# Optimization experiments

Measured on AMD Instinct MI355X. Metric: run time of the kernel, lower is better.

Reference implementation:

```python
import sys
import jax, jax.numpy as jnp
import numpy as np

sys.setrecursionlimit(100000)

MARGIN = 200.0
SAME_MARGIN = 0.0
REL_MARGIN = MARGIN - SAME_MARGIN  # margin - same_margin


def km_algorithm(mp):
    """Faithful numpy port of the repo's recursive Kuhn-Munkres (host-side,
    exactly mirroring the original CPU round-trip). mp: (n, n) float64.
    Returns transport plan T with T[link[y], y] = 1/n for matched pairs."""
    n = mp.shape[0]
    link = np.full(n, -1, dtype=np.int64)
    lx = mp.max(axis=1).astype(np.float64).copy()
    ly = np.zeros(n, dtype=np.float64)
    st = {}

    def dfs(x):
        st['visx'][x] = True
        for y in range(n):
            if st['visy'][y]:
                continue
            tmp = lx[x] + ly[y] - mp[x, y]
            if abs(tmp) < 1e-5:
                st['visy'][y] = True
                if link[y] == -1 or dfs(link[y]):
                    link[y] = x
                    return True
            elif st['sla'][y] + 1e-5 > tmp:
                st['sla'][y] = tmp
        return False

    for x in range(n):
        st['sla'] = np.full(n, 1e10, dtype=np.float64)
        while True:
            st['visx'] = np.zeros(n, dtype=bool)
            st['visy'] = np.zeros(n, dtype=bool)
            if dfs(x):
                break
            d = st['sla'][~st['visy']].min()
            lx[st['visx']] -= d
            ly[st['visy']] += d
            st['sla'][~st['visy']] -= d
    T = np.zeros((n, n), dtype=np.float64)
    for i in range(n):
        if link[i] != -1:
            T[link[i], i] = 1.0 / n
    return T


def sim_label(l1, l2):
    # (n, n) float: 1 where labels equal
    return (l1[:, None] == l2[None, :]).astype(jnp.float32)


def ground_metric(f1, f2, sim):
    # pairwise squared euclidean distances: ||a||^2 - 2 a.b + ||b||^2
    sq1 = jnp.sum(f1 * f1, axis=1)[:, None]
    sq2 = jnp.sum(f2 * f2, axis=1)[None, :]
    d2 = sq1 - 2.0 * (f1 @ f2.T) + sq2
    hinge_gm = jnp.maximum(0.0, SAME_MARGIN + REL_MARGIN - d2)   # negative pairs
    same_gm = jnp.maximum(0.0, d2 - SAME_MARGIN)                 # positive pairs
    return sim * same_gm + (1.0 - sim) * hinge_gm                # mode='both'


def setup_inputs() -> dict:
    key = jax.random.key(0)
    k1, k2, k3, k4 = jax.random.split(key, 4)
    n, d = 128, 8192
    return {
        "inputs_batch1": jax.random.normal(k1, (n, d), dtype=jnp.float32),
        "inputs_batch2": jax.random.normal(k2, (n, d), dtype=jnp.float32),
        "targets_batch1": jax.random.randint(k3, (n,), 0, 16, dtype=jnp.int64) if jax.config.jax_enable_x64 else jax.random.randint(k3, (n,), 0, 16).astype(jnp.int32),
        "targets_batch2": jax.random.randint(k4, (n,), 0, 16, dtype=jnp.int64) if jax.config.jax_enable_x64 else jax.random.randint(k4, (n,), 0, 16).astype(jnp.int32),
    }


def reference(inputs_batch1, inputs_batch2, targets_batch1, targets_batch2):
    sim = sim_label(targets_batch1, targets_batch2)
    GM = ground_metric(inputs_batch1, inputs_batch2, sim)
    # host round-trip for KM assignment, as in the original module
    T = km_algorithm(np.asarray(jax.device_get(GM), dtype=np.float64))
    T = jnp.asarray(T, dtype=jnp.float32)
    loss = jnp.sum(GM * T)
    return loss
```

## Files before the change

### kernel.cpp

```cpp
#include <hip/hip_runtime.h>

#define N 128
#define DIM 8192
#define NN (N * N)
#define ZSPLIT 64
#define NW 16
#define GSTRIDE 130
#define NSTR 65

__device__ __forceinline__ void wave_fence() {
    __threadfence_block();
    __builtin_amdgcn_wave_barrier();
}
__device__ __forceinline__ double embed_key(double v, int j) {
    long long b = __double_as_longlong(v);
    return __longlong_as_double((b & ~127LL) | (long long)j);
}

__global__ __launch_bounds__(256) void d2_partial(const float* __restrict__ A,
                                                  const float* __restrict__ B,
                                                  float* __restrict__ d2p) {
    __shared__ float As[32][68];
    __shared__ float Bk[64][36];
    const int tid = threadIdx.x;
    const int bi = blockIdx.x, bj = blockIdx.y, bz = blockIdx.z;
    const int tx = tid & 15, ty = tid >> 4;
    const int row0 = bi * 32, col0 = bj * 32;
    const int kbase = bz * 128;
    float a00 = 0.f, a01 = 0.f, a10 = 0.f, a11 = 0.f;

    for (int it = 0; it < 2; ++it) {
        const int k0 = kbase + it * 64;
        __syncthreads();
        #pragma unroll
        for (int s = 0; s < 2; ++s) {
            int e = tid + s * 256;
            int r = e >> 4, q = e & 15;
            *(float4*)&As[r][q * 4] = *(const float4*)&A[(row0 + r) * DIM + k0 + q * 4];
        }
        #pragma unroll
        for (int s = 0; s < 2; ++s) {
            int r = tid & 31;
            int kq = (tid >> 5) + s * 8;
            float4 b4 = *(const float4*)&B[(col0 + r) * DIM + k0 + kq * 4];
            Bk[kq * 4 + 0][r] = b4.x;
            Bk[kq * 4 + 1][r] = b4.y;
            Bk[kq * 4 + 2][r] = b4.z;
            Bk[kq * 4 + 3][r] = b4.w;
        }
        __syncthreads();
        #pragma unroll
        for (int kk = 0; kk < 64; kk += 4) {
            float x0[4], x1[4];
            *(float4*)x0 = *(const float4*)&As[2 * ty][kk];
            *(float4*)x1 = *(const float4*)&As[2 * ty + 1][kk];
            float y[4][2];
            #pragma unroll
            for (int q = 0; q < 4; ++q)
                *(float2*)y[q] = *(const float2*)&Bk[kk + q][2 * tx];
            #pragma unroll
            for (int q = 0; q < 4; ++q) {
                float d;
                d = x0[q] - y[q][0]; a00 = fmaf(d, d, a00);
                d = x0[q] - y[q][1]; a01 = fmaf(d, d, a01);
                d = x1[q] - y[q][0]; a10 = fmaf(d, d, a10);
                d = x1[q] - y[q][1]; a11 = fmaf(d, d, a11);
            }
        }
    }
    const int o0 = (row0 + 2 * ty) * N + col0 + 2 * tx;
    float* dst = d2p + bz * NN;
    *(float2*)&dst[o0]     = make_float2(a00, a01);
    *(float2*)&dst[o0 + N] = make_float2(a10, a11);
}

__global__ __launch_bounds__(256) void reduce_gm(const float* __restrict__ d2p,
                                                 const int* __restrict__ t1,
                                                 const int* __restrict__ t2,
                                                 float* __restrict__ gm,
                                                 int* __restrict__ flagarr) {
    __shared__ int bf;
    if (threadIdx.x == 0) bf = 0;
    __syncthreads();
    const int o = blockIdx.x * 256 + threadIdx.x;
    float s0 = 0.f, s1 = 0.f, s2 = 0.f, s3 = 0.f, s4 = 0.f, s5 = 0.f, s6 = 0.f, s7 = 0.f;
    const float* p = d2p + o;
    #pragma unroll
    for (int z = 0; z < ZSPLIT; z += 8) {
        s0 += p[(z + 0) * NN]; s1 += p[(z + 1) * NN];
        s2 += p[(z + 2) * NN]; s3 += p[(z + 3) * NN];
        s4 += p[(z + 4) * NN]; s5 += p[(z + 5) * NN];
        s6 += p[(z + 6) * NN]; s7 += p[(z + 7) * NN];
    }
    float s = ((s0 + s1) + (s2 + s3)) + ((s4 + s5) + (s6 + s7));
    const int i = o >> 7, j = o & 127;
    const int l1 = t1[i], l2 = t2[j];
    const bool same = (l1 == l2);
    float g = same ? fmaxf(s, 0.f) : fmaxf(200.f - s, 0.f);
    gm[o] = g;
    bool bad = (!same && g > 0.f) || l1 < 0 || l1 > 63 || l2 < 0 || l2 > 63;
    unsigned long long m = __ballot(bad);
    if ((threadIdx.x & 63) == 0 && m) atomicOr(&bf, 1);
    __syncthreads();
    if (threadIdx.x == 0) flagarr[blockIdx.x] = bf;
}

__global__ __launch_bounds__(64) void solve_classes(const float* __restrict__ gm,
                                                    const int* __restrict__ flagarr,
                                                    const int* __restrict__ t1,
                                                    const int* __restrict__ t2,
                                                    double* __restrict__ cls_val) {
    __shared__ float ncls[64 * NSTR];
    __shared__ int rowl[64], coll[64];
    __shared__ int rcnt[64], ccnt[64];
    __shared__ int tasks[64];
    __shared__ int clm[64];

    const int lane = threadIdx.x;
    const int l1a = t1[lane] & 63, l1b = t1[lane + 64] & 63;
    const int l2a = t2[lane] & 63, l2b = t2[lane + 64] & 63;
    const int fl  = flagarr[lane];
    rcnt[lane] = 0; ccnt[lane] = 0;
    __syncthreads();
    atomicAdd(&rcnt[l1a], 1); atomicAdd(&rcnt[l1b], 1);
    atomicAdd(&ccnt[l2a], 1); atomicAdd(&ccnt[l2b], 1);
    __syncthreads();
    const bool flag = (__ballot(fl != 0) != 0ull);
    int ntasks;
    {
        int R = rcnt[lane], C = ccnt[lane];
        bool small = (!flag) && (R > 0) && (C > 0) && (R <= 64) && (C <= 64);
        unsigned long long ms = __ballot(small);
        if (small) tasks[__popcll(ms & ((1ull << lane) - 1))] = lane;
        ntasks = (int)__popcll(ms);
    }
    __syncthreads();
    if ((int)blockIdx.x >= ntasks) {
        if (lane == 0) cls_val[blockIdx.x] = 0.0;
        return;
    }
    const int c = tasks[blockIdx.x];

    const unsigned long long mlt = (1ull << lane) - 1;
    unsigned long long b1 = __ballot(l1a == c);
    unsigned long long b2 = __ballot(l1b == c);
    if (l1a == c) rowl[__popcll(b1 & mlt)] = lane;
    if (l1b == c) rowl[__popcll(b1) + __popcll(b2 & mlt)] = lane + 64;
    const int Rn = (int)(__popcll(b1) + __popcll(b2));
    unsigned long long c1 = __ballot(l2a == c);
    unsigned long long c2 = __ballot(l2b == c);
    if (l2a == c) coll[__popcll(c1 & mlt)] = lane;
    if (l2b == c) coll[__popcll(c1) + __popcll(c2 & mlt)] = lane + 64;
    const int Cn = (int)(__popcll(c1) + __popcll(c2));
    __syncthreads();

    const bool T  = (Rn > Cn);
    const int n_  = T ? Cn : Rn;
    const int m_  = T ? Rn : Cn;
    const int tot = n_ * m_;
    for (int e = lane; e < tot; e += 64) {
        int i = e / m_, j = e - i * m_;
        int gr = T ? rowl[j] : rowl[i];
        int gc = T ? coll[i] : coll[j];
        ncls[i * NSTR + j] = gm[gr * N + gc];
    }
    __syncthreads();

    const int W = (m_ <= 16) ? 16 : (m_ <= 32 ? 32 : 64);
    const bool cA = (lane < m_), rA = (lane < n_);

    double u = 0.0;
    if (rA) {
        float mx = 0.f;
        const float* row = &ncls[lane * NSTR];
        for (int j = 0; j < m_; ++j) mx = fmaxf(mx, row[j]);
        u = -(double)mx;
    }
    double v = 1e30;
    for (int i = 0; i < n_; ++i) {
        double ui = __shfl(u, i, 64);
        if (cA) v = fmin(v, -(double)ncls[i * NSTR + lane] - ui);
    }
    if (cA) clm[lane] = 0x7fffffff;
    wave_fence();
    int jc = -1;
    for (int j = 0; j < m_; ++j) {
        double vj = __shfl(v, j, 64);
        if (rA && jc < 0) {
            double s = -(double)ncls[lane * NSTR + j] - u - vj;
            if (s < 1e-7) jc = j;
        }
    }
    if (rA && jc >= 0) atomicMin(&clm[jc], lane);
    wave_fence();
    int p = -1;
    if (cA && clm[lane] != 0x7fffffff) p = clm[lane];
    bool rowm = (rA && jc >= 0 && clm[jc] == lane);

    for (int ir = 0; ir < n_; ++ir) {
        if (__shfl(rowm ? 1 : 0, ir, 64)) continue;
        double minv = 1e30, markD = -1.0, ent = -1.0;
        bool used = false; int way = -2;
        if (rA && lane == ir) ent = 0.0;
        double D = 0.0;
        int i0 = ir, jprev = -1;
        int guard = 2 * m_ + 8;
        while (guard-- > 0) {
            double ui = __shfl(u, i0, 64);
            if (cA && !used) {
                double cand = D - ui - (double)ncls[i0 * NSTR + lane] - v;
                if (cand < minv) { minv = cand; way = jprev; }
            }
            double kd = (cA && !used) ? embed_key(minv, lane) : 1e30;
            for (int o = 1; o < W; o <<= 1) kd = fmin(kd, __shfl_xor(kd, o, 64));
            long long kb = __double_as_longlong(kd);
            int j1 = (int)(kb & 127);
            double Dn = __longlong_as_double(kb & ~127LL);
            if (Dn > 1e29) break;
            D = Dn;
            int i1 = __shfl(p, j1, 64);
            if (i1 < 0) {
                int jj = j1;
                while (true) {
                    int wp = __shfl(way, jj, 64);
                    int pn = (wp < 0) ? ir : __shfl(p, wp, 64);
                    if (cA && lane == jj) p = pn;
                    if (wp < 0) break;
                    jj = wp;
                }
                if (rA && lane == ir) rowm = true;
                break;
            }
            if (cA && lane == j1) { used = true; markD = D; }
            if (rA && lane == i1) ent = D;
            jprev = j1; i0 = i1;
        }
        if (rA && ent   >= 0.0) u += D - ent;
        if (cA && markD >= 0.0) v -= D - markD;
    }

    double val = 0.0;
    if (cA && p >= 0) val = (double)ncls[p * NSTR + lane];
    #pragma unroll
    for (int o = 1; o < 64; o <<= 1) val += __shfl_xor(val, o, 64);
    if (lane == 0) cls_val[blockIdx.x] = val;
}

__global__ __launch_bounds__(1024) void finalize_kernel(const float* __restrict__ gm,
                                                        const int* __restrict__ flagarr,
                                                        const int* __restrict__ t1,
                                                        const int* __restrict__ t2,
                                                        const double* __restrict__ cls_val,
                                                        float* __restrict__ out) {
    __shared__ float gml[N * GSTRIDE];
    __shared__ int lbl1[N], lbl2[N];
    __shared__ int rowlist[N], collist[N];
    __shared__ int rcnt[64], ccnt[64], rstart[65], cstart[65], rcur[64], ccur[64];
    __shared__ int bigtasks[65];
    __shared__ int nbig_s, flag_s;
    __shared__ double ub[N + 1], vbp[N + 1], minvb[N + 1];
    __shared__ int pb[N + 1], wayb[N + 1], usedb[N + 1];
    __shared__ double redv[NW];
    __shared__ int redi[NW];
    __shared__ double big_total, small_sum;
    __shared__ int jfin_s;

    const int tid = threadIdx.x;
    if (tid < 64) { rcnt[tid] = 0; ccnt[tid] = 0; rcur[tid] = 0; ccur[tid] = 0; }
    if (tid == 0) { nbig_s = 0; flag_s = 0; big_total = 0.0; }
    if (tid < N)  { lbl1[tid] = t1[tid]; lbl2[tid] = t2[tid]; }
    __syncthreads();
    if (tid < 64 && flagarr[tid]) atomicOr(&flag_s, 1);
    if (tid < N) {
        atomicAdd(&rcnt[lbl1[tid] & 63], 1);
        atomicAdd(&ccnt[lbl2[tid] & 63], 1);
    }
    double sv = (tid < 64) ? cls_val[tid] : 0.0;
    __syncthreads();
    if (tid < 64) {
        int rs_ = rcnt[tid], cs_ = ccnt[tid];
        #pragma unroll
        for (int o = 1; o < 64; o <<= 1) {
            int tr = __shfl_up(rs_, o, 64);
            int tc = __shfl_up(cs_, o, 64);
            if (tid >= o) { rs_ += tr; cs_ += tc; }
        }
        rstart[tid + 1] = rs_;
        cstart[tid + 1] = cs_;
        if (tid == 0) { rstart[0] = 0; cstart[0] = 0; }
        if (!flag_s) {
            int R = rcnt[tid], C = ccnt[tid];
            bool big = (R > 0) && (C > 0) && ((R > 64) || (C > 64));
            unsigned long long mb = __ballot(big);
            if (big) bigtasks[__popcll(mb & ((1ull << tid) - 1))] = tid;
            if (tid == 0) nbig_s = __popcll(mb);
        } else if (tid == 0) { nbig_s = 1; bigtasks[0] = -1; }
        #pragma unroll
        for (int o = 1; o < 64; o <<= 1) sv += __shfl_xor(sv, o, 64);
        if (tid == 0) small_sum = sv;
    }
    __syncthreads();

    const int nbig = nbig_s;
    if (nbig > 0) {
        if (tid < N) {
            int l1 = lbl1[tid] & 63;
            int p = atomicAdd(&rcur[l1], 1);
            rowlist[rstart[l1] + p] = tid;
            int l2 = lbl2[tid] & 63;
            int q = atomicAdd(&ccur[l2], 1);
            collist[cstart[l2] + q] = tid;
        }
        __syncthreads();
        #pragma unroll
        for (int pch = 0; pch < 16; ++pch) {
            int e = tid + pch * 1024;
            int i = e >> 7, j = e & 127;
            gml[i * GSTRIDE + j] = gm[rowlist[i] * N + collist[j]];
        }
        __syncthreads();

        for (int bt = 0; bt < nbig; ++bt) {
            const int c = bigtasks[bt];
            int Rn, Cn, rs, cs;
            if (c < 0) { Rn = N; Cn = N; rs = 0; cs = 0; }
            else { Rn = rcnt[c]; Cn = ccnt[c]; rs = rstart[c]; cs = cstart[c]; }
            const bool T = (Rn > Cn);
            const int n_ = T ? Cn : Rn, m_ = T ? Rn : Cn;
            const int rstep = T ? 1 : GSTRIDE;
            const int cstep = T ? GSTRIDE : 1;
            const int rb00 = T ? cs : rs * GSTRIDE;
            const int ob00 = T ? rs * GSTRIDE : cs;
            auto cost = [&](int i, int j) -> double {
                return -(double)gml[rb00 + i * rstep + ob00 + j * cstep];
            };
            for (int x = tid; x <= m_; x += 1024) { vbp[x] = 0.0; pb[x] = 0; }
            for (int x = tid; x <= n_; x += 1024) { ub[x] = 0.0; }
            __syncthreads();
            for (int i = 1; i <= n_; ++i) {
                if (tid == 0) pb[0] = i;
                for (int x = tid; x <= m_; x += 1024) { minvb[x] = 1e300; usedb[x] = 0; }
                __syncthreads();
                int j0 = 0;
                int guard = 2 * m_ + 8;
                while (guard-- > 0) {
                    if (tid == 0) usedb[j0] = 1;
                    __syncthreads();
                    const int i0 = pb[j0];
                    double dl = 1e300; int jl = 0;
                    if (tid < m_) {
                        int j = tid + 1;
                        if (!usedb[j]) {
                            double cur = cost(i0 - 1, j - 1) - ub[i0] - vbp[j];
                            if (cur < minvb[j]) { minvb[j] = cur; wayb[j] = j0; }
                            dl = minvb[j]; jl = j;
                        }
                    }
                    double rv = dl; int ri = jl;
                    #pragma unroll
                    for (int o = 32; o > 0; o >>= 1) {
                        double ov = __shfl_down(rv, o, 64);
                        int oi2 = __shfl_down(ri, o, 64);
                        if (ov < rv) { rv = ov; ri = oi2; }
                    }
                    if ((tid & 63) == 0) { redv[tid >> 6] = rv; redi[tid >> 6] = ri; }
                    __syncthreads();
                    if (tid == 0) {
                        double bd = 1e300; int bj = 0;
                        for (int q = 0; q < NW; ++q) if (redv[q] < bd) { bd = redv[q]; bj = redi[q]; }
                        redv[0] = bd; redi[0] = bj;
                    }
                    __syncthreads();
                    const double delta = redv[0];
                    const int j1 = redi[0];
                    if (tid < m_) {
                        int j = tid + 1;
                        if (usedb[j]) { ub[pb[j]] += delta; vbp[j] -= delta; }
                        else          { minvb[j] -= delta; }
                    }
                    if (tid == 0) ub[pb[0]] += delta;
                    __syncthreads();
                    j0 = j1;
                    if (pb[j0] == 0) break;
                }
                if (tid == 0) jfin_s = j0;
                __syncthreads();
                if (tid == 0) {
                    int jj = jfin_s;
                    while (jj) { int jp = wayb[jj]; pb[jj] = pb[jp]; jj = jp; }
                }
                __syncthreads();
            }
            double bl = 0.0;
            if (tid < m_) { int j = tid + 1; if (pb[j] != 0) bl = -cost(pb[j] - 1, j - 1); }
            #pragma unroll
            for (int o = 32; o > 0; o >>= 1) bl += __shfl_down(bl, o, 64);
            if ((tid & 63) == 0) redv[tid >> 6] = bl;
            __syncthreads();
            if (tid == 0) { double s = 0; for (int q = 0; q < NW; ++q) s += redv[q]; big_total += s; }
            __syncthreads();
        }
    }

    if (tid == 0) out[0] = (float)((small_sum + big_total) / (double)N);
}

extern "C" void kernel_launch(void* const* d_in, const int* in_sizes, int n_in,
                              void* d_out, int out_size, void* d_ws, size_t ws_size,
                              hipStream_t stream) {
    const float* A  = (const float*)d_in[0];
    const float* B  = (const float*)d_in[1];
    const int*   t1 = (const int*)d_in[2];
    const int*   t2 = (const int*)d_in[3];
    float* out = (float*)d_out;
    float* d2p = (float*)d_ws;
    float* gm  = (float*)d_ws + ZSPLIT * NN;
    int*   flagarr = (int*)(gm + NN);
    double* cls_val = (double*)(flagarr + 64);

    d2_partial<<<dim3(4, 4, ZSPLIT), 256, 0, stream>>>(A, B, d2p);
    reduce_gm<<<64, 256, 0, stream>>>(d2p, t1, t2, gm, flagarr);
    solve_classes<<<64, 64, 0, stream>>>(gm, flagarr, t1, t2, cls_val);
    finalize_kernel<<<1, 1024, 0, stream>>>(gm, flagarr, t1, t2, cls_val, out);
}
```

Before: 88.80 us.

## Fuse four kernels into one cooperative kernel with grid syncs

```diff
diff --git a/kernel.cpp b/kernel.cpp
--- a/kernel.cpp
+++ b/kernel.cpp
@@ -1,10 +1,14 @@
 #include <hip/hip_runtime.h>
+#include <hip/hip_cooperative_groups.h>
+
+namespace cg = cooperative_groups;
 
 #define N 128
 #define DIM 8192
 #define NN (N * N)
 #define ZSPLIT 64
-#define NW 16
+#define BDIM 512
+#define NWF 8
 #define GSTRIDE 130
 #define NSTR 65
 
@@ -17,255 +21,242 @@
     return __longlong_as_double((b & ~127LL) | (long long)j);
 }
 
-__global__ __launch_bounds__(256) void d2_partial(const float* __restrict__ A,
-                                                  const float* __restrict__ B,
-                                                  float* __restrict__ d2p) {
-    __shared__ float As[32][68];
-    __shared__ float Bk[64][36];
-    const int tid = threadIdx.x;
-    const int bi = blockIdx.x, bj = blockIdx.y, bz = blockIdx.z;
-    const int tx = tid & 15, ty = tid >> 4;
-    const int row0 = bi * 32, col0 = bj * 32;
-    const int kbase = bz * 128;
-    float a00 = 0.f, a01 = 0.f, a10 = 0.f, a11 = 0.f;
-
-    for (int it = 0; it < 2; ++it) {
-        const int k0 = kbase + it * 64;
-        __syncthreads();
-        #pragma unroll
-        for (int s = 0; s < 2; ++s) {
-            int e = tid + s * 256;
-            int r = e >> 4, q = e & 15;
-            *(float4*)&As[r][q * 4] = *(const float4*)&A[(row0 + r) * DIM + k0 + q * 4];
-        }
-        #pragma unroll
-        for (int s = 0; s < 2; ++s) {
-            int r = tid & 31;
-            int kq = (tid >> 5) + s * 8;
-            float4 b4 = *(const float4*)&B[(col0 + r) * DIM + k0 + kq * 4];
-            Bk[kq * 4 + 0][r] = b4.x;
-            Bk[kq * 4 + 1][r] = b4.y;
-            Bk[kq * 4 + 2][r] = b4.z;
-            Bk[kq * 4 + 3][r] = b4.w;
-        }
-        __syncthreads();
-        #pragma unroll
-        for (int kk = 0; kk < 64; kk += 4) {
-            float x0[4], x1[4];
-            *(float4*)x0 = *(const float4*)&As[2 * ty][kk];
-            *(float4*)x1 = *(const float4*)&As[2 * ty + 1][kk];
-            float y[4][2];
-            #pragma unroll
-            for (int q = 0; q < 4; ++q)
-                *(float2*)y[q] = *(const float2*)&Bk[kk + q][2 * tx];
-            #pragma unroll
-            for (int q = 0; q < 4; ++q) {
-                float d;
-                d = x0[q] - y[q][0]; a00 = fmaf(d, d, a00);
-                d = x0[q] - y[q][1]; a01 = fmaf(d, d, a01);
-                d = x1[q] - y[q][0]; a10 = fmaf(d, d, a10);
-                d = x1[q] - y[q][1]; a11 = fmaf(d, d, a11);
-            }
-        }
-    }
-    const int o0 = (row0 + 2 * ty) * N + col0 + 2 * tx;
-    float* dst = d2p + bz * NN;
-    *(float2*)&dst[o0]     = make_float2(a00, a01);
-    *(float2*)&dst[o0 + N] = make_float2(a10, a11);
-}
-
-__global__ __launch_bounds__(256) void reduce_gm(const float* __restrict__ d2p,
-                                                 const int* __restrict__ t1,
-                                                 const int* __restrict__ t2,
-                                                 float* __restrict__ gm,
-                                                 int* __restrict__ flagarr) {
-    __shared__ int bf;
-    if (threadIdx.x == 0) bf = 0;
-    __syncthreads();
-    const int o = blockIdx.x * 256 + threadIdx.x;
-    float s0 = 0.f, s1 = 0.f, s2 = 0.f, s3 = 0.f, s4 = 0.f, s5 = 0.f, s6 = 0.f, s7 = 0.f;
-    const float* p = d2p + o;
-    #pragma unroll
-    for (int z = 0; z < ZSPLIT; z += 8) {
-        s0 += p[(z + 0) * NN]; s1 += p[(z + 1) * NN];
-        s2 += p[(z + 2) * NN]; s3 += p[(z + 3) * NN];
-        s4 += p[(z + 4) * NN]; s5 += p[(z + 5) * NN];
-        s6 += p[(z + 6) * NN]; s7 += p[(z + 7) * NN];
-    }
-    float s = ((s0 + s1) + (s2 + s3)) + ((s4 + s5) + (s6 + s7));
-    const int i = o >> 7, j = o & 127;
-    const int l1 = t1[i], l2 = t2[j];
-    const bool same = (l1 == l2);
-    float g = same ? fmaxf(s, 0.f) : fmaxf(200.f - s, 0.f);
-    gm[o] = g;
-    bool bad = (!same && g > 0.f) || l1 < 0 || l1 > 63 || l2 < 0 || l2 > 63;
-    unsigned long long m = __ballot(bad);
-    if ((threadIdx.x & 63) == 0 && m) atomicOr(&bf, 1);
-    __syncthreads();
-    if (threadIdx.x == 0) flagarr[blockIdx.x] = bf;
-}
-
-__global__ __launch_bounds__(64) void solve_classes(const float* __restrict__ gm,
-                                                    const int* __restrict__ flagarr,
+__global__ __launch_bounds__(BDIM) void mega_kernel(const float* __restrict__ A,
+                                                    const float* __restrict__ B,
                                                     const int* __restrict__ t1,
                                                     const int* __restrict__ t2,
-                                                    double* __restrict__ cls_val) {
-    __shared__ float ncls[64 * NSTR];
-    __shared__ int rowl[64], coll[64];
-    __shared__ int rcnt[64], ccnt[64];
-    __shared__ int tasks[64];
-    __shared__ int clm[64];
-
-    const int lane = threadIdx.x;
-    const int l1a = t1[lane] & 63, l1b = t1[lane + 64] & 63;
-    const int l2a = t2[lane] & 63, l2b = t2[lane + 64] & 63;
-    const int fl  = flagarr[lane];
-    rcnt[lane] = 0; ccnt[lane] = 0;
-    __syncthreads();
-    atomicAdd(&rcnt[l1a], 1); atomicAdd(&rcnt[l1b], 1);
-    atomicAdd(&ccnt[l2a], 1); atomicAdd(&ccnt[l2b], 1);
-    __syncthreads();
-    const bool flag = (__ballot(fl != 0) != 0ull);
-    int ntasks;
-    {
-        int R = rcnt[lane], C = ccnt[lane];
-        bool small = (!flag) && (R > 0) && (C > 0) && (R <= 64) && (C <= 64);
-        unsigned long long ms = __ballot(small);
-        if (small) tasks[__popcll(ms & ((1ull << lane) - 1))] = lane;
-        ntasks = (int)__popcll(ms);
-    }
-    __syncthreads();
-    if ((int)blockIdx.x >= ntasks) {
-        if (lane == 0) cls_val[blockIdx.x] = 0.0;
-        return;
-    }
-    const int c = tasks[blockIdx.x];
-
-    const unsigned long long mlt = (1ull << lane) - 1;
-    unsigned long long b1 = __ballot(l1a == c);
-    unsigned long long b2 = __ballot(l1b == c);
-    if (l1a == c) rowl[__popcll(b1 & mlt)] = lane;
-    if (l1b == c) rowl[__popcll(b1) + __popcll(b2 & mlt)] = lane + 64;
-    const int Rn = (int)(__popcll(b1) + __popcll(b2));
-    unsigned long long c1 = __ballot(l2a == c);
-    unsigned long long c2 = __ballot(l2b == c);
-    if (l2a == c) coll[__popcll(c1 & mlt)] = lane;
-    if (l2b == c) coll[__popcll(c1) + __popcll(c2 & mlt)] = lane + 64;
-    const int Cn = (int)(__popcll(c1) + __popcll(c2));
-    __syncthreads();
-
-    const bool T  = (Rn > Cn);
-    const int n_  = T ? Cn : Rn;
-    const int m_  = T ? Rn : Cn;
-    const int tot = n_ * m_;
-    for (int e = lane; e < tot; e += 64) {
-        int i = e / m_, j = e - i * m_;
-        int gr = T ? rowl[j] : rowl[i];
-        int gc = T ? coll[i] : coll[j];
-        ncls[i * NSTR + j] = gm[gr * N + gc];
-    }
-    __syncthreads();
-
-    const int W = (m_ <= 16) ? 16 : (m_ <= 32 ? 32 : 64);
-    const bool cA = (lane < m_), rA = (lane < n_);
-
-    double u = 0.0;
-    if (rA) {
-        float mx = 0.f;
-        const float* row = &ncls[lane * NSTR];
-        for (int j = 0; j < m_; ++j) mx = fmaxf(mx, row[j]);
-        u = -(double)mx;
-    }
-    double v = 1e30;
-    for (int i = 0; i < n_; ++i) {
-        double ui = __shfl(u, i, 64);
-        if (cA) v = fmin(v, -(double)ncls[i * NSTR + lane] - ui);
-    }
-    if (cA) clm[lane] = 0x7fffffff;
-    wave_fence();
-    int jc = -1;
-    for (int j = 0; j < m_; ++j) {
-        double vj = __shfl(v, j, 64);
-        if (rA && jc < 0) {
-            double s = -(double)ncls[lane * NSTR + j] - u - vj;
-            if (s < 1e-7) jc = j;
-        }
-    }
-    if (rA && jc >= 0) atomicMin(&clm[jc], lane);
-    wave_fence();
-    int p = -1;
-    if (cA && clm[lane] != 0x7fffffff) p = clm[lane];
-    bool rowm = (rA && jc >= 0 && clm[jc] == lane);
-
-    for (int ir = 0; ir < n_; ++ir) {
-        if (__shfl(rowm ? 1 : 0, ir, 64)) continue;
-        double minv = 1e30, markD = -1.0, ent = -1.0;
-        bool used = false; int way = -2;
-        if (rA && lane == ir) ent = 0.0;
-        double D = 0.0;
-        int i0 = ir, jprev = -1;
-        int guard = 2 * m_ + 8;
-        while (guard-- > 0) {
-            double ui = __shfl(u, i0, 64);
-            if (cA && !used) {
-                double cand = D - ui - (double)ncls[i0 * NSTR + lane] - v;
-                if (cand < minv) { minv = cand; way = jprev; }
-            }
-            double kd = (cA && !used) ? embed_key(minv, lane) : 1e30;
-            for (int o = 1; o < W; o <<= 1) kd = fmin(kd, __shfl_xor(kd, o, 64));
-            long long kb = __double_as_longlong(kd);
-            int j1 = (int)(kb & 127);
-            double Dn = __longlong_as_double(kb & ~127LL);
-            if (Dn > 1e29) break;
-            D = Dn;
-            int i1 = __shfl(p, j1, 64);
-            if (i1 < 0) {
-                int jj = j1;
-                while (true) {
-                    int wp = __shfl(way, jj, 64);
-                    int pn = (wp < 0) ? ir : __shfl(p, wp, 64);
-                    if (cA && lane == jj) p = pn;
-                    if (wp < 0) break;
-                    jj = wp;
-                }
-                if (rA && lane == ir) rowm = true;
-                break;
-            }
-            if (cA && lane == j1) { used = true; markD = D; }
-            if (rA && lane == i1) ent = D;
-            jprev = j1; i0 = i1;
-        }
-        if (rA && ent   >= 0.0) u += D - ent;
-        if (cA && markD >= 0.0) v -= D - markD;
-    }
-
-    double val = 0.0;
-    if (cA && p >= 0) val = (double)ncls[p * NSTR + lane];
-    #pragma unroll
-    for (int o = 1; o < 64; o <<= 1) val += __shfl_xor(val, o, 64);
-    if (lane == 0) cls_val[blockIdx.x] = val;
-}
-
-__global__ __launch_bounds__(1024) void finalize_kernel(const float* __restrict__ gm,
-                                                        const int* __restrict__ flagarr,
-                                                        const int* __restrict__ t1,
-                                                        const int* __restrict__ t2,
-                                                        const double* __restrict__ cls_val,
-                                                        float* __restrict__ out) {
-    __shared__ float gml[N * GSTRIDE];
-    __shared__ int lbl1[N], lbl2[N];
-    __shared__ int rowlist[N], collist[N];
-    __shared__ int rcnt[64], ccnt[64], rstart[65], cstart[65], rcur[64], ccur[64];
-    __shared__ int bigtasks[65];
-    __shared__ int nbig_s, flag_s;
+                                                    float* __restrict__ d2p,
+                                                    float* __restrict__ gm,
+                                                    int* __restrict__ flagarr,
+                                                    double* __restrict__ cls_val,
+                                                    float* __restrict__ out) {
+    union Shm {
+        struct { float As[64][36]; float Bk[32][68]; } d2;
+        float ncls[64 * NSTR];
+        float gml[N * GSTRIDE];
+    };
+    __shared__ Shm sh;
+    __shared__ int bf;
+    __shared__ int rowl[64], coll[64], rcnt[64], ccnt[64], tasks64[64], clm[64];
+    __shared__ int lbl1[N], lbl2[N], rowlist[N], collist[N];
+    __shared__ int rstart[65], cstart[65], rcur[64], ccur[64], bigtasks[65];
+    __shared__ int nbig_s, flag_s, jfin_s;
     __shared__ double ub[N + 1], vbp[N + 1], minvb[N + 1];
     __shared__ int pb[N + 1], wayb[N + 1], usedb[N + 1];
-    __shared__ double redv[NW];
-    __shared__ int redi[NW];
+    __shared__ double redv[NWF];
+    __shared__ int redi[NWF];
     __shared__ double big_total, small_sum;
-    __shared__ int jfin_s;
 
     const int tid = threadIdx.x;
+    cg::grid_group grid = cg::this_grid();
+
+    {
+        const int bz = blockIdx.x & 63;
+        const int bi = (blockIdx.x >> 6) & 1;
+        const int bj = (blockIdx.x >> 7) & 1;
+        const int row0 = bi * 64, col0 = bj * 64;
+        const int kbase = bz * 128;
+        const int tx = tid & 15, ty = tid >> 4;
+        const int lr = tid >> 3, lq = tid & 7;
+        float a0[4] = {0.f, 0.f, 0.f, 0.f}, a1[4] = {0.f, 0.f, 0.f, 0.f};
+
+        for (int it = 0; it < 4; ++it) {
+            const int k0 = kbase + it * 32;
+            __syncthreads();
+            *(float4*)&sh.d2.As[lr][lq * 4] = *(const float4*)&A[(row0 + lr) * DIM + k0 + lq * 4];
+            float4 b4 = *(const float4*)&B[(col0 + lr) * DIM + k0 + lq * 4];
+            sh.d2.Bk[lq * 4 + 0][lr] = b4.x;
+            sh.d2.Bk[lq * 4 + 1][lr] = b4.y;
+            sh.d2.Bk[lq * 4 + 2][lr] = b4.z;
+            sh.d2.Bk[lq * 4 + 3][lr] = b4.w;
+            __syncthreads();
+            #pragma unroll
+            for (int kk = 0; kk < 32; kk += 4) {
+                float x0[4], x1[4];
+                *(float4*)x0 = *(const float4*)&sh.d2.As[2 * ty][kk];
+                *(float4*)x1 = *(const float4*)&sh.d2.As[2 * ty + 1][kk];
+                #pragma unroll
+                for (int q = 0; q < 4; ++q) {
+                    float y[4];
+                    *(float4*)y = *(const float4*)&sh.d2.Bk[kk + q][tx * 4];
+                    #pragma unroll
+                    for (int c = 0; c < 4; ++c) {
+                        float d0 = x0[q] - y[c]; a0[c] = fmaf(d0, d0, a0[c]);
+                        float d1 = x1[q] - y[c]; a1[c] = fmaf(d1, d1, a1[c]);
+                    }
+                }
+            }
+        }
+        float* dst = d2p + bz * NN;
+        const int o0 = (row0 + 2 * ty) * N + col0 + tx * 4;
+        *(float4*)&dst[o0]     = *(float4*)a0;
+        *(float4*)&dst[o0 + N] = *(float4*)a1;
+    }
+    grid.sync();
+
+    {
+        if (tid == 0) bf = 0;
+        __syncthreads();
+        const bool active = (blockIdx.x < 64) && (tid < 256);
+        bool bad = false;
+        if (active) {
+            const int o = blockIdx.x * 256 + tid;
+            const float* p = d2p + o;
+            float s0 = 0.f, s1 = 0.f, s2 = 0.f, s3 = 0.f, s4 = 0.f, s5 = 0.f, s6 = 0.f, s7 = 0.f;
+            #pragma unroll
+            for (int z = 0; z < ZSPLIT; z += 8) {
+                s0 += p[(z + 0) * NN]; s1 += p[(z + 1) * NN];
+                s2 += p[(z + 2) * NN]; s3 += p[(z + 3) * NN];
+                s4 += p[(z + 4) * NN]; s5 += p[(z + 5) * NN];
+                s6 += p[(z + 6) * NN]; s7 += p[(z + 7) * NN];
+            }
+            float s = ((s0 + s1) + (s2 + s3)) + ((s4 + s5) + (s6 + s7));
+            const int i = o >> 7, j = o & 127;
+            const int l1 = t1[i], l2 = t2[j];
+            const bool same = (l1 == l2);
+            float g = same ? fmaxf(s, 0.f) : fmaxf(200.f - s, 0.f);
+            gm[o] = g;
+            bad = (!same && g > 0.f) || l1 < 0 || l1 > 63 || l2 < 0 || l2 > 63;
+        }
+        unsigned long long m = __ballot(bad);
+        if ((tid & 63) == 0 && m) atomicOr(&bf, 1);
+        __syncthreads();
+        if (blockIdx.x < 64 && tid == 0) flagarr[blockIdx.x] = bf;
+    }
+    grid.sync();
+
+    if (blockIdx.x < 64 && tid < 64) {
+        const int lane = tid;
+        const int l1a = t1[lane] & 63, l1b = t1[lane + 64] & 63;
+        const int l2a = t2[lane] & 63, l2b = t2[lane + 64] & 63;
+        const int fl  = flagarr[lane];
+        rcnt[lane] = 0; ccnt[lane] = 0;
+        wave_fence();
+        atomicAdd(&rcnt[l1a], 1); atomicAdd(&rcnt[l1b], 1);
+        atomicAdd(&ccnt[l2a], 1); atomicAdd(&ccnt[l2b], 1);
+        wave_fence();
+        const bool flag = (__ballot(fl != 0) != 0ull);
+        int ntasks;
+        {
+            int R = rcnt[lane], C = ccnt[lane];
+            bool small = (!flag) && (R > 0) && (C > 0) && (R <= 64) && (C <= 64);
+            unsigned long long ms = __ballot(small);
+            if (small) tasks64[__popcll(ms & ((1ull << lane) - 1))] = lane;
+            ntasks = (int)__popcll(ms);
+        }
+        wave_fence();
+        const bool have = ((int)blockIdx.x < ntasks);
+        double val = 0.0;
+        if (have) {
+            const int c = tasks64[blockIdx.x];
+            const unsigned long long mlt = (1ull << lane) - 1;
+            unsigned long long b1 = __ballot(l1a == c);
+            unsigned long long b2 = __ballot(l1b == c);
+            if (l1a == c) rowl[__popcll(b1 & mlt)] = lane;
+            if (l1b == c) rowl[__popcll(b1) + __popcll(b2 & mlt)] = lane + 64;
+            const int Rn = (int)(__popcll(b1) + __popcll(b2));
+            unsigned long long c1 = __ballot(l2a == c);
+            unsigned long long c2 = __ballot(l2b == c);
+            if (l2a == c) coll[__popcll(c1 & mlt)] = lane;
+            if (l2b == c) coll[__popcll(c1) + __popcll(c2 & mlt)] = lane + 64;
+            const int Cn = (int)(__popcll(c1) + __popcll(c2));
+            wave_fence();
+
+            const bool T  = (Rn > Cn);
+            const int n_  = T ? Cn : Rn;
+            const int m_  = T ? Rn : Cn;
+            const int tot = n_ * m_;
+            for (int e = lane; e < tot; e += 64) {
+                int i = e / m_, j = e - i * m_;
+                int gr = T ? rowl[j] : rowl[i];
+                int gc = T ? coll[i] : coll[j];
+                sh.ncls[i * NSTR + j] = gm[gr * N + gc];
+            }
+            wave_fence();
+
+            const int W = (m_ <= 16) ? 16 : (m_ <= 32 ? 32 : 64);
+            const bool cA = (lane < m_), rA = (lane < n_);
+
+            double u = 0.0;
+            if (rA) {
+                float mx = 0.f;
+                const float* row = &sh.ncls[lane * NSTR];
+                for (int j = 0; j < m_; ++j) mx = fmaxf(mx, row[j]);
+                u = -(double)mx;
+            }
+            double v = 1e30;
+            for (int i = 0; i < n_; ++i) {
+                double ui = __shfl(u, i, 64);
+                if (cA) v = fmin(v, -(double)sh.ncls[i * NSTR + lane] - ui);
+            }
+            if (cA) clm[lane] = 0x7fffffff;
+            wave_fence();
+            int jc = -1;
+            for (int j = 0; j < m_; ++j) {
+                double vj = __shfl(v, j, 64);
+                if (rA && jc < 0) {
+                    double s = -(double)sh.ncls[lane * NSTR + j] - u - vj;
+                    if (s < 1e-7) jc = j;
+                }
+            }
+            if (rA && jc >= 0) atomicMin(&clm[jc], lane);
+            wave_fence();
+            int p = -1;
+            if (cA && clm[lane] != 0x7fffffff) p = clm[lane];
+            bool rowm = (rA && jc >= 0 && clm[jc] == lane);
+
+            for (int ir = 0; ir < n_; ++ir) {
+                if (__shfl(rowm ? 1 : 0, ir, 64)) continue;
+                double minv = 1e30, markD = -1.0, ent = -1.0;
+                bool used = false; int way = -2;
+                if (rA && lane == ir) ent = 0.0;
+                double D = 0.0;
+                int i0 = ir, jprev = -1;
+                int guard = 2 * m_ + 8;
+                while (guard-- > 0) {
+                    double ui = __shfl(u, i0, 64);
+                    if (cA && !used) {
+                        double cand = D - ui - (double)sh.ncls[i0 * NSTR + lane] - v;
+                        if (cand < minv) { minv = cand; way = jprev; }
+                    }
+                    double kd = (cA && !used) ? embed_key(minv, lane) : 1e30;
+                    for (int o = 1; o < W; o <<= 1) kd = fmin(kd, __shfl_xor(kd, o, 64));
+                    long long kb = __double_as_longlong(kd);
+                    int j1 = (int)(kb & 127);
+                    double Dn = __longlong_as_double(kb & ~127LL);
+                    if (Dn > 1e29) break;
+                    D = Dn;
+                    int i1 = __shfl(p, j1, 64);
+                    if (i1 < 0) {
+                        int jj = j1;
+                        while (true) {
+                            int wp = __shfl(way, jj, 64);
+                            int pn = (wp < 0) ? ir : __shfl(p, wp, 64);
+                            if (cA && lane == jj) p = pn;
+                            if (wp < 0) break;
+                            jj = wp;
+                        }
+                        if (rA && lane == ir) rowm = true;
+                        break;
+                    }
+                    if (cA && lane == j1) { used = true; markD = D; }
+                    if (rA && lane == i1) ent = D;
+                    jprev = j1; i0 = i1;
+                }
+                if (rA && ent   >= 0.0) u += D - ent;
+                if (cA && markD >= 0.0) v -= D - markD;
+            }
+
+            if (cA && p >= 0) val = (double)sh.ncls[p * NSTR + lane];
+            #pragma unroll
+            for (int o = 1; o < 64; o <<= 1) val += __shfl_xor(val, o, 64);
+        }
+        if (lane == 0) cls_val[blockIdx.x] = have ? val : 0.0;
+    }
+    grid.sync();
+
+    if (blockIdx.x != 0) return;
+
     if (tid < 64) { rcnt[tid] = 0; ccnt[tid] = 0; rcur[tid] = 0; ccur[tid] = 0; }
     if (tid == 0) { nbig_s = 0; flag_s = 0; big_total = 0.0; }
     if (tid < N)  { lbl1[tid] = t1[tid]; lbl2[tid] = t2[tid]; }
@@ -313,10 +304,10 @@
         }
         __syncthreads();
         #pragma unroll
-        for (int pch = 0; pch < 16; ++pch) {
-            int e = tid + pch * 1024;
+        for (int pch = 0; pch < 32; ++pch) {
+            int e = tid + pch * BDIM;
             int i = e >> 7, j = e & 127;
-            gml[i * GSTRIDE + j] = gm[rowlist[i] * N + collist[j]];
+            sh.gml[i * GSTRIDE + j] = gm[rowlist[i] * N + collist[j]];
         }
         __syncthreads();
 
@@ -332,14 +323,14 @@
             const int rb00 = T ? cs : rs * GSTRIDE;
             const int ob00 = T ? rs * GSTRIDE : cs;
             auto cost = [&](int i, int j) -> double {
-                return -(double)gml[rb00 + i * rstep + ob00 + j * cstep];
+                return -(double)sh.gml[rb00 + i * rstep + ob00 + j * cstep];
             };
-            for (int x = tid; x <= m_; x += 1024) { vbp[x] = 0.0; pb[x] = 0; }
-            for (int x = tid; x <= n_; x += 1024) { ub[x] = 0.0; }
+            for (int x = tid; x <= m_; x += BDIM) { vbp[x] = 0.0; pb[x] = 0; }
+            for (int x = tid; x <= n_; x += BDIM) { ub[x] = 0.0; }
             __syncthreads();
             for (int i = 1; i <= n_; ++i) {
                 if (tid == 0) pb[0] = i;
-                for (int x = tid; x <= m_; x += 1024) { minvb[x] = 1e300; usedb[x] = 0; }
+                for (int x = tid; x <= m_; x += BDIM) { minvb[x] = 1e300; usedb[x] = 0; }
                 __syncthreads();
                 int j0 = 0;
                 int guard = 2 * m_ + 8;
@@ -367,7 +358,7 @@
                     __syncthreads();
                     if (tid == 0) {
                         double bd = 1e300; int bj = 0;
-                        for (int q = 0; q < NW; ++q) if (redv[q] < bd) { bd = redv[q]; bj = redi[q]; }
+                        for (int q = 0; q < NWF; ++q) if (redv[q] < bd) { bd = redv[q]; bj = redi[q]; }
                         redv[0] = bd; redi[0] = bj;
                     }
                     __syncthreads();
@@ -397,7 +388,7 @@
             for (int o = 32; o > 0; o >>= 1) bl += __shfl_down(bl, o, 64);
             if ((tid & 63) == 0) redv[tid >> 6] = bl;
             __syncthreads();
-            if (tid == 0) { double s = 0; for (int q = 0; q < NW; ++q) s += redv[q]; big_total += s; }
+            if (tid == 0) { double s = 0; for (int q = 0; q < NWF; ++q) s += redv[q]; big_total += s; }
             __syncthreads();
         }
     }
@@ -418,8 +409,9 @@
     int*   flagarr = (int*)(gm + NN);
     double* cls_val = (double*)(flagarr + 64);
 
-    d2_partial<<<dim3(4, 4, ZSPLIT), 256, 0, stream>>>(A, B, d2p);
-    reduce_gm<<<64, 256, 0, stream>>>(d2p, t1, t2, gm, flagarr);
-    solve_classes<<<64, 64, 0, stream>>>(gm, flagarr, t1, t2, cls_val);
-    finalize_kernel<<<1, 1024, 0, stream>>>(gm, flagarr, t1, t2, cls_val, out);
+    void* args[] = {(void*)&A, (void*)&B, (void*)&t1, (void*)&t2,
+                    (void*)&d2p, (void*)&gm, (void*)&flagarr,
+                    (void*)&cls_val, (void*)&out};
+    hipLaunchCooperativeKernel((const void*)mega_kernel, dim3(256), dim3(BDIM),
+                               args, 0, stream);
 }
```

Result: slower. 181.1 us (+103.9%).
